# Performance work log

Measured on AMD Instinct MI355X. Metric: run time of the kernel, lower is better.

Reference implementation:

```python
import jax, jax.numpy as jnp
import numpy as np

N_GAUSS = 1024
IMG_H = 128
IMG_W = 128
FOV_HALF = np.pi / 6.0  # 60 deg FOV
MIN_ALPHA = 1.0 / 255.0


def setup_inputs() -> dict:
    key = jax.random.key(0)
    k1, k2, k3, k4, k5 = jax.random.split(key, 5)
    # Gaussians placed in front of an identity camera looking down +z
    xy = jax.random.uniform(k1, (N_GAUSS, 2), minval=-3.0, maxval=3.0)
    z = jax.random.uniform(k2, (N_GAUSS, 1), minval=3.0, maxval=8.0)
    positions = jnp.concatenate([xy, z], axis=1).astype(jnp.float32)
    # PSD world-space covariances: A A^T + eps I
    A = jax.random.normal(k3, (N_GAUSS, 3, 3), dtype=jnp.float32) * 0.1
    covariances = jnp.einsum('nij,nkj->nik', A, A) + 0.01 * jnp.eye(3, dtype=jnp.float32)
    colors = jax.random.uniform(k4, (N_GAUSS, 3), dtype=jnp.float32)
    opacities = jax.random.uniform(k5, (N_GAUSS,), dtype=jnp.float32)
    camera_matrix = jnp.eye(4, dtype=jnp.float32)
    return {
        'positions': positions,
        'covariances': covariances,
        'colors': colors,
        'opacities': opacities,
        'camera_matrix': camera_matrix,
        'height': IMG_H,
        'width': IMG_W,
    }


def reference(positions, covariances, colors, opacities, camera_matrix, height, width):
    H, W = height, width
    focal = jnp.float32(0.5 * W / np.tan(FOV_HALF))
    # --- preprocess: project to camera space ---
    R = camera_matrix[:3, :3]
    t = camera_matrix[:3, 3]
    p_cam = positions @ R.T + t  # (N,3)
    x, y, z = p_cam[:, 0], p_cam[:, 1], p_cam[:, 2]
    zc = jnp.maximum(z, 1e-6)
    means_x = focal * x / zc + 0.5 * W
    means_y = focal * y / zc + 0.5 * H
    # perspective Jacobian (N,2,3) for EWA splatting
    zeros = jnp.zeros_like(zc)
    J = jnp.stack([
        jnp.stack([focal / zc, zeros, -focal * x / (zc * zc)], axis=-1),
        jnp.stack([zeros, focal / zc, -focal * y / (zc * zc)], axis=-1),
    ], axis=-2)
    covs = 0.5 * (covariances + jnp.swapaxes(covariances, -1, -2))
    cov_cam = jnp.einsum('ij,njk,lk->nil', R, covs, R)      # (N,3,3)
    cov2d = jnp.einsum('nij,njk,nlk->nil', J, cov_cam, J)   # (N,2,2)
    cov2d = cov2d + 0.3 * jnp.eye(2, dtype=cov2d.dtype)      # low-pass filter (3DGS)
    a = cov2d[:, 0, 0]; b = cov2d[:, 0, 1]; c = cov2d[:, 1, 1]
    det = a * c - b * b
    det_safe = jnp.where(det > 0, det, 1.0)
    conic_a = c / det_safe
    conic_b = -b / det_safe
    conic_c = a / det_safe
    valid = (z > 0.2) & (det > 0)
    # --- sort front-to-back by depth ---
    order = jnp.argsort(z)
    mx = means_x[order]; my = means_y[order]
    ca = conic_a[order]; cb = conic_b[order]; cc = conic_c[order]
    op = opacities[order]; col = colors[order]; vld = valid[order]
    # --- render: per-pixel alpha compositing (Algorithm 1) ---
    px = jnp.arange(W, dtype=jnp.float32) + 0.5
    py = jnp.arange(H, dtype=jnp.float32) + 0.5
    dx = px[None, None, :] - mx[:, None, None]  # (N,1,W)
    dy = py[None, :, None] - my[:, None, None]  # (N,H,1)
    power = -0.5 * (ca[:, None, None] * dx * dx + cc[:, None, None] * dy * dy) \
            - cb[:, None, None] * dx * dy        # (N,H,W)
    G = jnp.exp(jnp.minimum(power, 0.0))
    alpha = jnp.clip(op[:, None, None] * G, 0.0, 0.99)
    alpha = jnp.where(vld[:, None, None] & (alpha >= MIN_ALPHA), alpha, 0.0)
    # exclusive transmittance T_i = prod_{j<i} (1 - alpha_j)
    T = jnp.cumprod(1.0 - alpha, axis=0)
    T_excl = jnp.concatenate([jnp.ones((1, H, W), dtype=alpha.dtype), T[:-1]], axis=0)
    wgt = alpha * T_excl                          # (N,H,W)
    image = jnp.einsum('nhw,nc->hwc', wgt, col)   # (H,W,3)
    return image
```

## Files before the change

### kernel.cpp

```cpp
#include <hip/hip_runtime.h>
#include <math.h>

#define NG      1024
#define IMG_H   128
#define IMG_W   128
#define NPIX    (IMG_H * IMG_W)
#define MIN_A   (1.0f / 255.0f)
#define LOG2E   1.4426950408889634f


__global__ __launch_bounds__(1024) void gs_prep(
    const float* __restrict__ pos, const float* __restrict__ cov,
    const float* __restrict__ col, const float* __restrict__ opa,
    const float* __restrict__ cm,
    float4* __restrict__ g0, float4* __restrict__ g1, float* __restrict__ g2,
    float4* __restrict__ g3)
{
    __shared__ float possh[NG * 3];
    __shared__ float zsh[NG];
    __shared__ float covsh[64 * 9];
    __shared__ float colsh[64 * 3];
    __shared__ float opash[64];
    __shared__ int   prank[16][64];

    const int tid = threadIdx.x;
    const int b   = blockIdx.x;

    if      (tid < 768) ((float4*)possh)[tid]       = ((const float4*)pos)[tid];
    else if (tid < 912) ((float4*)covsh)[tid - 768] = ((const float4*)cov)[144 * b + tid - 768];
    else if (tid < 960) ((float4*)colsh)[tid - 912] = ((const float4*)col)[48 * b + tid - 912];
    else if (tid < 976) ((float4*)opash)[tid - 960] = ((const float4*)opa)[16 * b + tid - 960];
    __syncthreads();

    const float R20 = cm[8], R21 = cm[9], R22 = cm[10], T2 = cm[11];
    zsh[tid] = fmaf(R20, possh[3*tid],
               fmaf(R21, possh[3*tid+1],
               fmaf(R22, possh[3*tid+2], T2)));
    __syncthreads();

    {
        const int q = tid >> 6, g = tid & 63;
        const int i = (b << 6) + g;
        const float zi = zsh[i];
        const float4* z4 = (const float4*)zsh;
        int r = 0;
        #pragma unroll
        for (int j4 = q * 16; j4 < q * 16 + 16; ++j4) {
            const float4 v = z4[j4];
            const int j = 4 * j4;
            r += (v.x < zi || (v.x == zi && j + 0 < i)) ? 1 : 0;
            r += (v.y < zi || (v.y == zi && j + 1 < i)) ? 1 : 0;
            r += (v.z < zi || (v.z == zi && j + 2 < i)) ? 1 : 0;
            r += (v.w < zi || (v.w == zi && j + 3 < i)) ? 1 : 0;
        }
        prank[q][g] = r;
    }
    __syncthreads();

    if (tid < 64) {
        const int g = tid;
        const int i = (b << 6) + g;

        const float R00 = cm[0], R01 = cm[1], R02 = cm[2],  T0 = cm[3];
        const float R10 = cm[4], R11 = cm[5], R12 = cm[6],  T1 = cm[7];

        const float p0 = possh[3*i], p1 = possh[3*i+1], p2 = possh[3*i+2];
        const float x = R00*p0 + R01*p1 + R02*p2 + T0;
        const float y = R10*p0 + R11*p1 + R12*p2 + T1;
        const float z = zsh[i];

        const float focal = 110.85125168440814f;
        const float zc = fmaxf(z, 1e-6f);
        const float mx = focal * x / zc + 0.5f * IMG_W;
        const float my = focal * y / zc + 0.5f * IMG_H;

        const float c00 = covsh[9*g+0], c01 = covsh[9*g+1], c02 = covsh[9*g+2];
        const float c10 = covsh[9*g+3], c11 = covsh[9*g+4], c12 = covsh[9*g+5];
        const float c20 = covsh[9*g+6], c21 = covsh[9*g+7], c22 = covsh[9*g+8];
        const float s00 = c00, s01 = 0.5f*(c01+c10), s02 = 0.5f*(c02+c20);
        const float s11 = c11, s12 = 0.5f*(c12+c21), s22 = c22;

        const float RS00 = R00*s00 + R01*s01 + R02*s02;
        const float RS01 = R00*s01 + R01*s11 + R02*s12;
        const float RS02 = R00*s02 + R01*s12 + R02*s22;
        const float RS10 = R10*s00 + R11*s01 + R12*s02;
        const float RS11 = R10*s01 + R11*s11 + R12*s12;
        const float RS12 = R10*s02 + R11*s12 + R12*s22;
        const float RS20 = R20*s00 + R21*s01 + R22*s02;
        const float RS21 = R20*s01 + R21*s11 + R22*s12;
        const float RS22 = R20*s02 + R21*s12 + R22*s22;
        const float CC00 = RS00*R00 + RS01*R01 + RS02*R02;
        const float CC01 = RS00*R10 + RS01*R11 + RS02*R12;
        const float CC02 = RS00*R20 + RS01*R21 + RS02*R22;
        const float CC11 = RS10*R10 + RS11*R11 + RS12*R12;
        const float CC12 = RS10*R20 + RS11*R21 + RS12*R22;
        const float CC20 = RS20*R00 + RS21*R01 + RS22*R02;
        const float CC21 = RS20*R10 + RS21*R11 + RS22*R12;
        const float CC22 = RS20*R20 + RS21*R21 + RS22*R22;

        const float j00 = focal / zc, j02 = -focal * x / (zc*zc);
        const float j11 = focal / zc, j12 = -focal * y / (zc*zc);

        const float v00 = CC00*j00 + CC02*j02;
        const float v02 = CC20*j00 + CC22*j02;
        const float v10 = CC01*j11 + CC02*j12;
        const float v11 = CC11*j11 + CC12*j12;
        const float v12 = CC21*j11 + CC22*j12;

        const float a  = j00*v00 + j02*v02 + 0.3f;
        const float bq = j00*v10 + j02*v12;
        const float cQ = j11*v11 + j12*v12 + 0.3f;

        const float det = a*cQ - bq*bq;
        const float det_safe = (det > 0.f) ? det : 1.f;
        const float conA =  cQ / det_safe;
        const float conB = -bq / det_safe;
        const float conC =  a  / det_safe;

        const bool  valid  = (z > 0.2f) && (det > 0.f);
        const float op_eff = valid ? opash[g] : 0.f;

        float dxm, dym;
        if (op_eff * 255.f > 1.f) {
            const float sN = logf(255.f * op_eff);
            dxm = sqrtf(2.f * sN * a)  * 1.001f + 0.06f;
            dym = sqrtf(2.f * sN * cQ) * 1.001f + 0.06f;
        } else {
            dxm = -1e30f; dym = -1e30f;
        }

        const int rank = prank[0][g]  + prank[1][g]  + prank[2][g]  + prank[3][g]
                       + prank[4][g]  + prank[5][g]  + prank[6][g]  + prank[7][g]
                       + prank[8][g]  + prank[9][g]  + prank[10][g] + prank[11][g]
                       + prank[12][g] + prank[13][g] + prank[14][g] + prank[15][g];

        g0[rank] = make_float4(mx, my, -0.5f*conA*LOG2E, -conB*LOG2E);
        g1[rank] = make_float4(-0.5f*conC*LOG2E, op_eff, colsh[3*g], colsh[3*g+1]);
        g2[rank] = colsh[3*g+2];
        g3[rank] = make_float4(mx, my, dxm, dym);
    }
}

__global__ __launch_bounds__(1024) void gs_raster_tile(
    const float4* __restrict__ g0, const float4* __restrict__ g1,
    const float*  __restrict__ g2, const float4* __restrict__ g3,
    float* __restrict__ out)
{
    __shared__ float4 s0[NG];
    __shared__ float4 s1[NG];
    __shared__ float  s2[NG];
    __shared__ float4 part[16][64];

    const int tid = threadIdx.x;
    const float4 cl = g3[tid];
    s0[tid] = g0[tid];
    s1[tid] = g1[tid];
    s2[tid] = g2[tid];

    const int w    = tid >> 6;
    const int lane = tid & 63;
    const int tile = blockIdx.x;
    const float tx0 = (float)((tile & 15) << 3);
    const float ty0 = (float)((tile >> 4) << 3);

    const float pxf = tx0 + (float)(lane & 7) + 0.5f;
    const float pyf = ty0 + (float)(lane >> 3) + 0.5f;
    const float txl = tx0 + 0.5f, txh = tx0 + 7.5f;
    const float tyl = ty0 + 0.5f, tyh = ty0 + 7.5f;

    const bool hit = (cl.x - cl.z <= txh) && (cl.x + cl.z >= txl)
                  && (cl.y - cl.w <= tyh) && (cl.y + cl.w >= tyl);
    unsigned long long m = __ballot(hit);

    __syncthreads();

    const int base = w * 64;
    float T = 1.f, cr = 0.f, cg = 0.f, cb = 0.f;

    while (m) {
        const int i = __builtin_ctzll(m);
        m &= m - 1;
        const float4 A = s0[base + i];
        const float4 B = s1[base + i];
        const float  C = s2[base + i];
        const float dx = pxf - A.x;
        const float dy = pyf - A.y;
        const float pw = fminf(A.z*dx*dx + B.x*dy*dy + A.w*(dx*dy), 0.f);
        const float G = __builtin_amdgcn_exp2f(pw);
        float alpha = fminf(B.y * G, 0.99f);
        alpha = (alpha >= MIN_A) ? alpha : 0.f;
        const float wT = alpha * T;
        cr = fmaf(wT, B.z, cr);
        cg = fmaf(wT, B.w, cg);
        cb = fmaf(wT, C,   cb);
        T *= (1.f - alpha);
    }

    part[w][lane] = make_float4(cr, cg, cb, T);
    __syncthreads();

    if (tid < 64) {
        float Ts = 1.f, r = 0.f, g = 0.f, b = 0.f;
        #pragma unroll
        for (int k = 0; k < 16; ++k) {
            const float4 v = part[k][tid];
            r = fmaf(Ts, v.x, r);
            g = fmaf(Ts, v.y, g);
            b = fmaf(Ts, v.z, b);
            Ts *= v.w;
        }
        const int px = (int)tx0 + (tid & 7);
        const int py = (int)ty0 + (tid >> 3);
        float* o = out + 3 * (py * IMG_W + px);
        o[0] = r; o[1] = g; o[2] = b;
    }
}

extern "C" void kernel_launch(void* const* d_in, const int* in_sizes, int n_in,
                              void* d_out, int out_size, void* d_ws, size_t ws_size,
                              hipStream_t stream) {
    const float* pos = (const float*)d_in[0];
    const float* cov = (const float*)d_in[1];
    const float* col = (const float*)d_in[2];
    const float* opa = (const float*)d_in[3];
    const float* cm  = (const float*)d_in[4];

    char* ws = (char*)d_ws;
    float4* g0 = (float4*)(ws);
    float4* g1 = (float4*)(ws + 16384);
    float*  g2 = (float*) (ws + 32768);
    float4* g3 = (float4*)(ws + 36864);

    gs_prep<<<16, 1024, 0, stream>>>(pos, cov, col, opa, cm, g0, g1, g2, g3);
    gs_raster_tile<<<256, 1024, 0, stream>>>(g0, g1, g2, g3, (float*)d_out);
}
```

Measured before the change: 14.03 us.

## Spread preprocessing over 64 blocks and drop shared-memory staging

The prep kernel now runs 64 blocks of 16 Gaussians each instead of 16 blocks of 64, and each thread's rank count scans 16 depths rather than 64. The shared-memory staging of positions, covariances, colors and opacities is removed; those values are read straight from global memory, which takes one barrier out of the prep kernel. The aim is a shorter prep critical path through more blocks and less serial work per thread. In exchange only 16 threads per block do the projection, the final rank sum adds 64 shared values serially, and the global reads are uncoalesced.

```diff
diff --git a/kernel.cpp b/kernel.cpp
--- a/kernel.cpp
+++ b/kernel.cpp
@@ -16,36 +16,27 @@
     float4* __restrict__ g0, float4* __restrict__ g1, float* __restrict__ g2,
     float4* __restrict__ g3)
 {
-    __shared__ float possh[NG * 3];
     __shared__ float zsh[NG];
-    __shared__ float covsh[64 * 9];
-    __shared__ float colsh[64 * 3];
-    __shared__ float opash[64];
-    __shared__ int   prank[16][64];
+    __shared__ int   prank[64][16];
 
     const int tid = threadIdx.x;
     const int b   = blockIdx.x;
 
-    if      (tid < 768) ((float4*)possh)[tid]       = ((const float4*)pos)[tid];
-    else if (tid < 912) ((float4*)covsh)[tid - 768] = ((const float4*)cov)[144 * b + tid - 768];
-    else if (tid < 960) ((float4*)colsh)[tid - 912] = ((const float4*)col)[48 * b + tid - 912];
-    else if (tid < 976) ((float4*)opash)[tid - 960] = ((const float4*)opa)[16 * b + tid - 960];
-    __syncthreads();
-
     const float R20 = cm[8], R21 = cm[9], R22 = cm[10], T2 = cm[11];
-    zsh[tid] = fmaf(R20, possh[3*tid],
-               fmaf(R21, possh[3*tid+1],
-               fmaf(R22, possh[3*tid+2], T2)));
-    __syncthreads();
-
     {
-        const int q = tid >> 6, g = tid & 63;
-        const int i = (b << 6) + g;
+        const float p0 = pos[3*tid], p1 = pos[3*tid+1], p2 = pos[3*tid+2];
+        zsh[tid] = fmaf(R20, p0, fmaf(R21, p1, fmaf(R22, p2, T2)));
+    }
+    __syncthreads();
+
+    {
+        const int g = tid & 15, q = tid >> 4;
+        const int i = (b << 4) + g;
         const float zi = zsh[i];
         const float4* z4 = (const float4*)zsh;
         int r = 0;
         #pragma unroll
-        for (int j4 = q * 16; j4 < q * 16 + 16; ++j4) {
+        for (int j4 = q * 4; j4 < q * 4 + 4; ++j4) {
             const float4 v = z4[j4];
             const int j = 4 * j4;
             r += (v.x < zi || (v.x == zi && j + 0 < i)) ? 1 : 0;
@@ -57,14 +48,18 @@
     }
     __syncthreads();
 
-    if (tid < 64) {
+    if (tid < 16) {
         const int g = tid;
-        const int i = (b << 6) + g;
+        const int i = (b << 4) + g;
+
+        int rank = 0;
+        #pragma unroll
+        for (int q = 0; q < 64; ++q) rank += prank[q][g];
 
         const float R00 = cm[0], R01 = cm[1], R02 = cm[2],  T0 = cm[3];
         const float R10 = cm[4], R11 = cm[5], R12 = cm[6],  T1 = cm[7];
 
-        const float p0 = possh[3*i], p1 = possh[3*i+1], p2 = possh[3*i+2];
+        const float p0 = pos[3*i], p1 = pos[3*i+1], p2 = pos[3*i+2];
         const float x = R00*p0 + R01*p1 + R02*p2 + T0;
         const float y = R10*p0 + R11*p1 + R12*p2 + T1;
         const float z = zsh[i];
@@ -74,9 +69,9 @@
         const float mx = focal * x / zc + 0.5f * IMG_W;
         const float my = focal * y / zc + 0.5f * IMG_H;
 
-        const float c00 = covsh[9*g+0], c01 = covsh[9*g+1], c02 = covsh[9*g+2];
-        const float c10 = covsh[9*g+3], c11 = covsh[9*g+4], c12 = covsh[9*g+5];
-        const float c20 = covsh[9*g+6], c21 = covsh[9*g+7], c22 = covsh[9*g+8];
+        const float c00 = cov[9*i+0], c01 = cov[9*i+1], c02 = cov[9*i+2];
+        const float c10 = cov[9*i+3], c11 = cov[9*i+4], c12 = cov[9*i+5];
+        const float c20 = cov[9*i+6], c21 = cov[9*i+7], c22 = cov[9*i+8];
         const float s00 = c00, s01 = 0.5f*(c01+c10), s02 = 0.5f*(c02+c20);
         const float s11 = c11, s12 = 0.5f*(c12+c21), s22 = c22;
 
@@ -118,7 +113,7 @@
         const float conC =  a  / det_safe;
 
         const bool  valid  = (z > 0.2f) && (det > 0.f);
-        const float op_eff = valid ? opash[g] : 0.f;
+        const float op_eff = valid ? opa[i] : 0.f;
 
         float dxm, dym;
         if (op_eff * 255.f > 1.f) {
@@ -129,14 +124,9 @@
             dxm = -1e30f; dym = -1e30f;
         }
 
-        const int rank = prank[0][g]  + prank[1][g]  + prank[2][g]  + prank[3][g]
-                       + prank[4][g]  + prank[5][g]  + prank[6][g]  + prank[7][g]
-                       + prank[8][g]  + prank[9][g]  + prank[10][g] + prank[11][g]
-                       + prank[12][g] + prank[13][g] + prank[14][g] + prank[15][g];
-
         g0[rank] = make_float4(mx, my, -0.5f*conA*LOG2E, -conB*LOG2E);
-        g1[rank] = make_float4(-0.5f*conC*LOG2E, op_eff, colsh[3*g], colsh[3*g+1]);
-        g2[rank] = colsh[3*g+2];
+        g1[rank] = make_float4(-0.5f*conC*LOG2E, op_eff, col[3*i], col[3*i+1]);
+        g2[rank] = col[3*i+2];
         g3[rank] = make_float4(mx, my, dxm, dym);
     }
 }
@@ -231,6 +221,6 @@
     float*  g2 = (float*) (ws + 32768);
     float4* g3 = (float4*)(ws + 36864);
 
-    gs_prep<<<16, 1024, 0, stream>>>(pos, cov, col, opa, cm, g0, g1, g2, g3);
+    gs_prep<<<64, 1024, 0, stream>>>(pos, cov, col, opa, cm, g0, g1, g2, g3);
     gs_raster_tile<<<256, 1024, 0, stream>>>(g0, g1, g2, g3, (float*)d_out);
 }
```

After: 13.17 us, median of 2. -6.1%, faster.
